# Kernel optimization log

Hardware: AMD Instinct MI355X
Metric: run time of the kernel (lower is better)

The kernel has to match this reference:

```python
import jax, jax.numpy as jnp
import numpy as np

N_NODES = 100_000
N_EDGES = 1_600_000
D_IN = 128
D_OUT = 128


def setup_inputs() -> dict:
    key = jax.random.key(0)
    k1, k2, k3, k4, k5 = jax.random.split(key, 5)
    feature = jax.random.normal(k1, (N_NODES, D_IN), dtype=jnp.float32)
    W = jax.random.normal(k2, (D_IN, D_OUT), dtype=jnp.float32) * 0.05
    b = jax.random.normal(k3, (D_OUT,), dtype=jnp.float32) * 0.05
    src = jax.random.randint(k4, (N_EDGES,), 0, N_NODES, dtype=jnp.int32)
    dst = jax.random.randint(k5, (N_EDGES,), 0, N_NODES, dtype=jnp.int32)
    return {"feature": feature, "W": W, "b": b, "src": src, "dst": dst}


def reference(feature, W, b, src, dst):
    N = feature.shape[0]
    # in-degrees (number of incoming edges per node)
    in_deg = jax.ops.segment_sum(
        jnp.ones(dst.shape[0], dtype=feature.dtype), dst, num_segments=N
    )  # [N]
    # degree-constraint scaling: h = x / sqrt(in_deg + 1)
    feat = feature * (1.0 / jnp.sqrt(in_deg + 1.0))[:, None]  # [N, D]
    # copy_u messages + mean reduce over incoming edges
    msg = feat[src]  # [E, D]
    summed = jax.ops.segment_sum(msg, dst, num_segments=N)  # [N, D]
    cnt = in_deg[:, None]
    h = jnp.where(cnt > 0, summed / jnp.maximum(cnt, 1.0), 0.0)  # DGL mean -> 0 for isolated nodes
    # apply_mod linear
    return h @ W + b
```

## Files before the change

kernel.cpp:

```cpp
#include <hip/hip_runtime.h>
#include <math.h>


#define D 128
#define MT 32
#define CPAD 16
#define INL 15
#define CAPT 48
#define SCAP 33

typedef short short8 __attribute__((ext_vector_type(8)));
typedef float f32x4 __attribute__((ext_vector_type(4)));

__device__ inline unsigned short f2b(float f) {
    unsigned u = __float_as_uint(f);
    return (unsigned short)((u + 0x7FFFu + ((u >> 16) & 1u)) >> 16);
}
#define B2F(u) __uint_as_float(((unsigned)(u)) << 16)

__global__ __launch_bounds__(256) void k_fill(const int* __restrict__ src,
                                              const int* __restrict__ dst,
                                              int* __restrict__ cl,
                                              int* __restrict__ spill,
                                              int ne, int nn) {
#define PUT(s_, d_) { int p = atomicAdd(&cl[(d_) * CPAD], 1);                  \
        if (p < INL) cl[(d_) * CPAD + 1 + p] = (s_);                           \
        else if (p < CAPT) spill[(size_t)(d_) * SCAP + (p - INL)] = (s_); }
    int i = blockIdx.x * 256 + threadIdx.x;
    int e0 = i * 4;
    if (e0 + 4 <= ne) {
        int4 sv = ((const int4*)src)[i];
        int4 dv = ((const int4*)dst)[i];
        PUT(sv.x, dv.x)
        PUT(sv.y, dv.y)
        PUT(sv.z, dv.z)
        PUT(sv.w, dv.w)
    } else {
        for (int e = e0; e < ne; ++e) PUT(src[e], dst[e])
    }
#undef PUT
}

__global__ __launch_bounds__(256) void k_mid(const int* __restrict__ cl,
                                             const float* __restrict__ W,
                                             float* __restrict__ scale,
                                             unsigned short* __restrict__ Wt,
                                             int nn, int sb) {
    int t = threadIdx.x;
    if (blockIdx.x < sb) {
        int n = blockIdx.x * 256 + t;
        if (n < nn) scale[n] = rsqrtf((float)cl[n * CPAD] + 1.0f);
        return;
    }
    int d = t & 127, k0 = (t >> 7) * 64;
    for (int k = 0; k < 64; ++k)
        Wt[d * D + k0 + k] = f2b(W[(size_t)(k0 + k) * D + d]);
}

__global__ __launch_bounds__(256) void k_gemm(const float* __restrict__ feature,
                                              const unsigned short* __restrict__ Wt,
                                              unsigned short* __restrict__ Yb,
                                              int nn) {
    int t = threadIdx.x;
    int w = t >> 6, l = t & 63;
    int rg = w & 1, ch = w >> 1;
    int base = blockIdx.x * MT;
    int r = base + rg * 16 + (l & 15);
    if (r >= nn) r = nn - 1;
    int kl = (l >> 4) * 8;

    short8 af[4];
    const float* fr = feature + (size_t)r * D;
#pragma unroll
    for (int kc = 0; kc < 4; ++kc) {
        float4 x = *(const float4*)(fr + kc * 32 + kl);
        float4 y = *(const float4*)(fr + kc * 32 + kl + 4);
        short8 a;
        a[0] = (short)f2b(x.x); a[1] = (short)f2b(x.y);
        a[2] = (short)f2b(x.z); a[3] = (short)f2b(x.w);
        a[4] = (short)f2b(y.x); a[5] = (short)f2b(y.y);
        a[6] = (short)f2b(y.z); a[7] = (short)f2b(y.w);
        af[kc] = a;
    }

    f32x4 acc[4];
#pragma unroll
    for (int ct = 0; ct < 4; ++ct) acc[ct] = (f32x4){0.f, 0.f, 0.f, 0.f};

#pragma unroll
    for (int ct = 0; ct < 4; ++ct) {
        int c = ch * 64 + ct * 16 + (l & 15);
        const unsigned short* wr = Wt + (size_t)c * D;
#pragma unroll
        for (int kc = 0; kc < 4; ++kc) {
            short8 b = *(const short8*)(wr + kc * 32 + kl);
            acc[ct] = __builtin_amdgcn_mfma_f32_16x16x32_bf16(af[kc], b, acc[ct], 0, 0, 0);
        }
    }

#pragma unroll
    for (int ct = 0; ct < 4; ++ct) {
        int c = ch * 64 + ct * 16 + (l & 15);
        int r0 = base + rg * 16 + (l >> 4) * 4;
#pragma unroll
        for (int j = 0; j < 4; ++j) {
            int row = r0 + j;
            if (row < nn) Yb[(size_t)row * D + c] = f2b(acc[ct][j]);
        }
    }
}

__global__ __launch_bounds__(256) void k_agg(const unsigned short* __restrict__ Yb,
                                             const float* __restrict__ bias,
                                             const int* __restrict__ cl,
                                             const int* __restrict__ spill,
                                             const float* __restrict__ scale,
                                             float* __restrict__ out,
                                             int n_nodes) {
    int t = threadIdx.x;
    int wave = t >> 6, lane = t & 63;
    int hw = lane >> 5, sl = lane & 31;
    int base = blockIdx.x * MT;

    const ushort4* y4 = (const ushort4*)Yb;
    float4 bv = ((const float4*)bias)[sl];

#pragma unroll
    for (int j = 0; j < 4; ++j) {
        int n = base + wave * 8 + j * 2 + hw;
        bool valid = (n < n_nodes);
        int nc = valid ? n : 0;
        int lv;
        if (sl < 16) lv = cl[nc * CPAD + sl];
        else         lv = spill[(size_t)nc * SCAP + (sl - 16)];
        int c = __shfl(lv, 0, 32);
        if (!valid) c = 0;
        if (c > CAPT) c = CAPT;
        float4 a0 = make_float4(0.f, 0.f, 0.f, 0.f), a1 = a0, a2 = a0, a3 = a0;
        if (c > 0) {
            int iv0 = ((unsigned)lv < (unsigned)n_nodes) ? lv : 0;
            float sv0 = scale[iv0];
            int nv = c < 31 ? c : 31;
            int e = 0;
            for (; e + 8 <= nv; e += 8) {
                int i0 = __shfl(iv0, e + 1, 32), i1 = __shfl(iv0, e + 2, 32);
                int i2 = __shfl(iv0, e + 3, 32), i3 = __shfl(iv0, e + 4, 32);
                int i4 = __shfl(iv0, e + 5, 32), i5 = __shfl(iv0, e + 6, 32);
                int i6 = __shfl(iv0, e + 7, 32), i7 = __shfl(iv0, e + 8, 32);
                float c0 = __shfl(sv0, e + 1, 32), c1 = __shfl(sv0, e + 2, 32);
                float c2 = __shfl(sv0, e + 3, 32), c3 = __shfl(sv0, e + 4, 32);
                float c4 = __shfl(sv0, e + 5, 32), c5 = __shfl(sv0, e + 6, 32);
                float c6 = __shfl(sv0, e + 7, 32), c7 = __shfl(sv0, e + 8, 32);
                ushort4 u0 = y4[(size_t)i0 * 32 + sl], u1 = y4[(size_t)i1 * 32 + sl];
                ushort4 u2 = y4[(size_t)i2 * 32 + sl], u3 = y4[(size_t)i3 * 32 + sl];
                ushort4 u4 = y4[(size_t)i4 * 32 + sl], u5 = y4[(size_t)i5 * 32 + sl];
                ushort4 u6 = y4[(size_t)i6 * 32 + sl], u7 = y4[(size_t)i7 * 32 + sl];
                a0.x = fmaf(B2F(u0.x), c0, a0.x); a0.y = fmaf(B2F(u0.y), c0, a0.y);
                a0.z = fmaf(B2F(u0.z), c0, a0.z); a0.w = fmaf(B2F(u0.w), c0, a0.w);
                a1.x = fmaf(B2F(u1.x), c1, a1.x); a1.y = fmaf(B2F(u1.y), c1, a1.y);
                a1.z = fmaf(B2F(u1.z), c1, a1.z); a1.w = fmaf(B2F(u1.w), c1, a1.w);
                a2.x = fmaf(B2F(u2.x), c2, a2.x); a2.y = fmaf(B2F(u2.y), c2, a2.y);
                a2.z = fmaf(B2F(u2.z), c2, a2.z); a2.w = fmaf(B2F(u2.w), c2, a2.w);
                a3.x = fmaf(B2F(u3.x), c3, a3.x); a3.y = fmaf(B2F(u3.y), c3, a3.y);
                a3.z = fmaf(B2F(u3.z), c3, a3.z); a3.w = fmaf(B2F(u3.w), c3, a3.w);
                a0.x = fmaf(B2F(u4.x), c4, a0.x); a0.y = fmaf(B2F(u4.y), c4, a0.y);
                a0.z = fmaf(B2F(u4.z), c4, a0.z); a0.w = fmaf(B2F(u4.w), c4, a0.w);
                a1.x = fmaf(B2F(u5.x), c5, a1.x); a1.y = fmaf(B2F(u5.y), c5, a1.y);
                a1.z = fmaf(B2F(u5.z), c5, a1.z); a1.w = fmaf(B2F(u5.w), c5, a1.w);
                a2.x = fmaf(B2F(u6.x), c6, a2.x); a2.y = fmaf(B2F(u6.y), c6, a2.y);
                a2.z = fmaf(B2F(u6.z), c6, a2.z); a2.w = fmaf(B2F(u6.w), c6, a2.w);
                a3.x = fmaf(B2F(u7.x), c7, a3.x); a3.y = fmaf(B2F(u7.y), c7, a3.y);
                a3.z = fmaf(B2F(u7.z), c7, a3.z); a3.w = fmaf(B2F(u7.w), c7, a3.w);
            }
            for (; e + 4 <= nv; e += 4) {
                int i0 = __shfl(iv0, e + 1, 32), i1 = __shfl(iv0, e + 2, 32);
                int i2 = __shfl(iv0, e + 3, 32), i3 = __shfl(iv0, e + 4, 32);
                float c0 = __shfl(sv0, e + 1, 32), c1 = __shfl(sv0, e + 2, 32);
                float c2 = __shfl(sv0, e + 3, 32), c3 = __shfl(sv0, e + 4, 32);
                ushort4 u0 = y4[(size_t)i0 * 32 + sl], u1 = y4[(size_t)i1 * 32 + sl];
                ushort4 u2 = y4[(size_t)i2 * 32 + sl], u3 = y4[(size_t)i3 * 32 + sl];
                a0.x = fmaf(B2F(u0.x), c0, a0.x); a0.y = fmaf(B2F(u0.y), c0, a0.y);
                a0.z = fmaf(B2F(u0.z), c0, a0.z); a0.w = fmaf(B2F(u0.w), c0, a0.w);
                a1.x = fmaf(B2F(u1.x), c1, a1.x); a1.y = fmaf(B2F(u1.y), c1, a1.y);
                a1.z = fmaf(B2F(u1.z), c1, a1.z); a1.w = fmaf(B2F(u1.w), c1, a1.w);
                a2.x = fmaf(B2F(u2.x), c2, a2.x); a2.y = fmaf(B2F(u2.y), c2, a2.y);
                a2.z = fmaf(B2F(u2.z), c2, a2.z); a2.w = fmaf(B2F(u2.w), c2, a2.w);
                a3.x = fmaf(B2F(u3.x), c3, a3.x); a3.y = fmaf(B2F(u3.y), c3, a3.y);
                a3.z = fmaf(B2F(u3.z), c3, a3.z); a3.w = fmaf(B2F(u3.w), c3, a3.w);
            }
            for (; e < nv; ++e) {
                int s = __shfl(iv0, e + 1, 32);
                float cc = __shfl(sv0, e + 1, 32);
                ushort4 u = y4[(size_t)s * 32 + sl];
                a0.x = fmaf(B2F(u.x), cc, a0.x); a0.y = fmaf(B2F(u.y), cc, a0.y);
                a0.z = fmaf(B2F(u.z), cc, a0.z); a0.w = fmaf(B2F(u.w), cc, a0.w);
            }
            for (int p = 31; p < c; ++p) {
                int s = spill[(size_t)nc * SCAP + (p - INL)];
                s = ((unsigned)s < (unsigned)n_nodes) ? s : 0;
                float cc = scale[s];
                ushort4 u = y4[(size_t)s * 32 + sl];
                a0.x = fmaf(B2F(u.x), cc, a0.x); a0.y = fmaf(B2F(u.y), cc, a0.y);
                a0.z = fmaf(B2F(u.z), cc, a0.z); a0.w = fmaf(B2F(u.w), cc, a0.w);
            }
        }
        if (valid) {
            float invn = (c > 0) ? (1.0f / (float)c) : 0.f;
            float4 r;
            r.x = (a0.x + a1.x + a2.x + a3.x) * invn + bv.x;
            r.y = (a0.y + a1.y + a2.y + a3.y) * invn + bv.y;
            r.z = (a0.z + a1.z + a2.z + a3.z) * invn + bv.z;
            r.w = (a0.w + a1.w + a2.w + a3.w) * invn + bv.w;
            ((float4*)out)[(size_t)n * 32 + sl] = r;
        }
    }
}

extern "C" void kernel_launch(void* const* d_in, const int* in_sizes, int n_in,
                              void* d_out, int out_size, void* d_ws, size_t ws_size,
                              hipStream_t stream) {
    const float* feature = (const float*)d_in[0];
    const float* W = (const float*)d_in[1];
    const float* bias = (const float*)d_in[2];
    const int* src = (const int*)d_in[3];
    const int* dst = (const int*)d_in[4];
    float* out = (float*)d_out;

    int n_nodes = in_sizes[0] / D;
    int n_edges = in_sizes[3];
    (void)n_in; (void)out_size; (void)ws_size;

    char* ws = (char*)d_ws;
    size_t o = 0;
    auto alloc = [&](size_t bytes) { void* p = ws + o; o += (bytes + 511) & ~(size_t)511; return p; };
    int* cl = (int*)alloc((size_t)n_nodes * CPAD * 4);
    int* spill = (int*)alloc((size_t)n_nodes * SCAP * 4);
    unsigned short* Yb = (unsigned short*)alloc((size_t)n_nodes * D * 2);
    float* scale = (float*)alloc((size_t)n_nodes * 4);
    unsigned short* Wt = (unsigned short*)alloc((size_t)D * D * 2);

    hipMemsetAsync(cl, 0, (size_t)n_nodes * CPAD * 4, stream);

    int fb = (n_edges + 1023) / 1024;
    int sb = (n_nodes + 255) / 256;
    int tiles = (n_nodes + MT - 1) / MT;

    k_fill<<<fb, 256, 0, stream>>>(src, dst, cl, spill, n_edges, n_nodes);
    k_mid<<<sb + 1, 256, 0, stream>>>(cl, W, scale, Wt, n_nodes, sb);
    k_gemm<<<tiles, 256, 0, stream>>>(feature, Wt, Yb, n_nodes);
    k_agg<<<tiles, 256, 0, stream>>>(Yb, bias, cl, spill, scale, out, n_nodes);
}
```

Before: 291.0 us.

## Fold source-degree scaling into GEMM epilogue and drop per-edge scale gathers

Moves the 1/sqrt(in_deg+1) source scaling out of the aggregation loop and applies it to each row of Y in the GEMM epilogue, using the linearity of the matmul. Aggregation then does plain bf16 adds with no per-edge scale gather or shuffle, the scale array and its kernel pass go away, and spill-list loads are skipped for low-degree nodes. In exchange the scale is applied before bf16 rounding of Y, which changes rounding slightly, and k_gemm now has to read the count array.

```diff
diff --git a/kernel.cpp b/kernel.cpp
--- a/kernel.cpp
+++ b/kernel.cpp
@@ -41,17 +41,9 @@
 #undef PUT
 }
 
-__global__ __launch_bounds__(256) void k_mid(const int* __restrict__ cl,
-                                             const float* __restrict__ W,
-                                             float* __restrict__ scale,
-                                             unsigned short* __restrict__ Wt,
-                                             int nn, int sb) {
+__global__ __launch_bounds__(256) void k_mid(const float* __restrict__ W,
+                                             unsigned short* __restrict__ Wt) {
     int t = threadIdx.x;
-    if (blockIdx.x < sb) {
-        int n = blockIdx.x * 256 + t;
-        if (n < nn) scale[n] = rsqrtf((float)cl[n * CPAD] + 1.0f);
-        return;
-    }
     int d = t & 127, k0 = (t >> 7) * 64;
     for (int k = 0; k < 64; ++k)
         Wt[d * D + k0 + k] = f2b(W[(size_t)(k0 + k) * D + d]);
@@ -59,6 +51,7 @@
 
 __global__ __launch_bounds__(256) void k_gemm(const float* __restrict__ feature,
                                               const unsigned short* __restrict__ Wt,
+                                              const int* __restrict__ cl,
                                               unsigned short* __restrict__ Yb,
                                               int nn) {
     int t = threadIdx.x;
@@ -98,14 +91,21 @@
         }
     }
 
+    int r0 = base + rg * 16 + (l >> 4) * 4;
+    float sc[4];
+#pragma unroll
+    for (int j = 0; j < 4; ++j) {
+        int row = (r0 + j < nn) ? (r0 + j) : (nn - 1);
+        sc[j] = rsqrtf((float)cl[row * CPAD] + 1.0f);
+    }
+
 #pragma unroll
     for (int ct = 0; ct < 4; ++ct) {
         int c = ch * 64 + ct * 16 + (l & 15);
-        int r0 = base + rg * 16 + (l >> 4) * 4;
 #pragma unroll
         for (int j = 0; j < 4; ++j) {
             int row = r0 + j;
-            if (row < nn) Yb[(size_t)row * D + c] = f2b(acc[ct][j]);
+            if (row < nn) Yb[(size_t)row * D + c] = f2b(acc[ct][j] * sc[j]);
         }
     }
 }
@@ -114,7 +114,6 @@
                                              const float* __restrict__ bias,
                                              const int* __restrict__ cl,
                                              const int* __restrict__ spill,
-                                             const float* __restrict__ scale,
                                              float* __restrict__ out,
                                              int n_nodes) {
     int t = threadIdx.x;
@@ -130,16 +129,15 @@
         int n = base + wave * 8 + j * 2 + hw;
         bool valid = (n < n_nodes);
         int nc = valid ? n : 0;
-        int lv;
-        if (sl < 16) lv = cl[nc * CPAD + sl];
-        else         lv = spill[(size_t)nc * SCAP + (sl - 16)];
+        int lv = cl[nc * CPAD + (sl & 15)];
         int c = __shfl(lv, 0, 32);
         if (!valid) c = 0;
         if (c > CAPT) c = CAPT;
+        if (c > INL && sl >= 16)
+            lv = spill[(size_t)nc * SCAP + (sl - 16)];
         float4 a0 = make_float4(0.f, 0.f, 0.f, 0.f), a1 = a0, a2 = a0, a3 = a0;
         if (c > 0) {
             int iv0 = ((unsigned)lv < (unsigned)n_nodes) ? lv : 0;
-            float sv0 = scale[iv0];
             int nv = c < 31 ? c : 31;
             int e = 0;
             for (; e + 8 <= nv; e += 8) {
@@ -147,61 +145,39 @@
                 int i2 = __shfl(iv0, e + 3, 32), i3 = __shfl(iv0, e + 4, 32);
                 int i4 = __shfl(iv0, e + 5, 32), i5 = __shfl(iv0, e + 6, 32);
                 int i6 = __shfl(iv0, e + 7, 32), i7 = __shfl(iv0, e + 8, 32);
-                float c0 = __shfl(sv0, e + 1, 32), c1 = __shfl(sv0, e + 2, 32);
-                float c2 = __shfl(sv0, e + 3, 32), c3 = __shfl(sv0, e + 4, 32);
-                float c4 = __shfl(sv0, e + 5, 32), c5 = __shfl(sv0, e + 6, 32);
-                float c6 = __shfl(sv0, e + 7, 32), c7 = __shfl(sv0, e + 8, 32);
                 ushort4 u0 = y4[(size_t)i0 * 32 + sl], u1 = y4[(size_t)i1 * 32 + sl];
                 ushort4 u2 = y4[(size_t)i2 * 32 + sl], u3 = y4[(size_t)i3 * 32 + sl];
                 ushort4 u4 = y4[(size_t)i4 * 32 + sl], u5 = y4[(size_t)i5 * 32 + sl];
                 ushort4 u6 = y4[(size_t)i6 * 32 + sl], u7 = y4[(size_t)i7 * 32 + sl];
-                a0.x = fmaf(B2F(u0.x), c0, a0.x); a0.y = fmaf(B2F(u0.y), c0, a0.y);
-                a0.z = fmaf(B2F(u0.z), c0, a0.z); a0.w = fmaf(B2F(u0.w), c0, a0.w);
-                a1.x = fmaf(B2F(u1.x), c1, a1.x); a1.y = fmaf(B2F(u1.y), c1, a1.y);
-                a1.z = fmaf(B2F(u1.z), c1, a1.z); a1.w = fmaf(B2F(u1.w), c1, a1.w);
-                a2.x = fmaf(B2F(u2.x), c2, a2.x); a2.y = fmaf(B2F(u2.y), c2, a2.y);
-                a2.z = fmaf(B2F(u2.z), c2, a2.z); a2.w = fmaf(B2F(u2.w), c2, a2.w);
-                a3.x = fmaf(B2F(u3.x), c3, a3.x); a3.y = fmaf(B2F(u3.y), c3, a3.y);
-                a3.z = fmaf(B2F(u3.z), c3, a3.z); a3.w = fmaf(B2F(u3.w), c3, a3.w);
-                a0.x = fmaf(B2F(u4.x), c4, a0.x); a0.y = fmaf(B2F(u4.y), c4, a0.y);
-                a0.z = fmaf(B2F(u4.z), c4, a0.z); a0.w = fmaf(B2F(u4.w), c4, a0.w);
-                a1.x = fmaf(B2F(u5.x), c5, a1.x); a1.y = fmaf(B2F(u5.y), c5, a1.y);
-                a1.z = fmaf(B2F(u5.z), c5, a1.z); a1.w = fmaf(B2F(u5.w), c5, a1.w);
-                a2.x = fmaf(B2F(u6.x), c6, a2.x); a2.y = fmaf(B2F(u6.y), c6, a2.y);
-                a2.z = fmaf(B2F(u6.z), c6, a2.z); a2.w = fmaf(B2F(u6.w), c6, a2.w);
-                a3.x = fmaf(B2F(u7.x), c7, a3.x); a3.y = fmaf(B2F(u7.y), c7, a3.y);
-                a3.z = fmaf(B2F(u7.z), c7, a3.z); a3.w = fmaf(B2F(u7.w), c7, a3.w);
+                a0.x += B2F(u0.x); a0.y += B2F(u0.y); a0.z += B2F(u0.z); a0.w += B2F(u0.w);
+                a1.x += B2F(u1.x); a1.y += B2F(u1.y); a1.z += B2F(u1.z); a1.w += B2F(u1.w);
+                a2.x += B2F(u2.x); a2.y += B2F(u2.y); a2.z += B2F(u2.z); a2.w += B2F(u2.w);
+                a3.x += B2F(u3.x); a3.y += B2F(u3.y); a3.z += B2F(u3.z); a3.w += B2F(u3.w);
+                a0.x += B2F(u4.x); a0.y += B2F(u4.y); a0.z += B2F(u4.z); a0.w += B2F(u4.w);
+                a1.x += B2F(u5.x); a1.y += B2F(u5.y); a1.z += B2F(u5.z); a1.w += B2F(u5.w);
+                a2.x += B2F(u6.x); a2.y += B2F(u6.y); a2.z += B2F(u6.z); a2.w += B2F(u6.w);
+                a3.x += B2F(u7.x); a3.y += B2F(u7.y); a3.z += B2F(u7.z); a3.w += B2F(u7.w);
             }
             for (; e + 4 <= nv; e += 4) {
                 int i0 = __shfl(iv0, e + 1, 32), i1 = __shfl(iv0, e + 2, 32);
                 int i2 = __shfl(iv0, e + 3, 32), i3 = __shfl(iv0, e + 4, 32);
-                float c0 = __shfl(sv0, e + 1, 32), c1 = __shfl(sv0, e + 2, 32);
-                float c2 = __shfl(sv0, e + 3, 32), c3 = __shfl(sv0, e + 4, 32);
                 ushort4 u0 = y4[(size_t)i0 * 32 + sl], u1 = y4[(size_t)i1 * 32 + sl];
                 ushort4 u2 = y4[(size_t)i2 * 32 + sl], u3 = y4[(size_t)i3 * 32 + sl];
-                a0.x = fmaf(B2F(u0.x), c0, a0.x); a0.y = fmaf(B2F(u0.y), c0, a0.y);
-                a0.z = fmaf(B2F(u0.z), c0, a0.z); a0.w = fmaf(B2F(u0.w), c0, a0.w);
-                a1.x = fmaf(B2F(u1.x), c1, a1.x); a1.y = fmaf(B2F(u1.y), c1, a1.y);
-                a1.z = fmaf(B2F(u1.z), c1, a1.z); a1.w = fmaf(B2F(u1.w), c1, a1.w);
-                a2.x = fmaf(B2F(u2.x), c2, a2.x); a2.y = fmaf(B2F(u2.y), c2, a2.y);
-                a2.z = fmaf(B2F(u2.z), c2, a2.z); a2.w = fmaf(B2F(u2.w), c2, a2.w);
-                a3.x = fmaf(B2F(u3.x), c3, a3.x); a3.y = fmaf(B2F(u3.y), c3, a3.y);
-                a3.z = fmaf(B2F(u3.z), c3, a3.z); a3.w = fmaf(B2F(u3.w), c3, a3.w);
+                a0.x += B2F(u0.x); a0.y += B2F(u0.y); a0.z += B2F(u0.z); a0.w += B2F(u0.w);
+                a1.x += B2F(u1.x); a1.y += B2F(u1.y); a1.z += B2F(u1.z); a1.w += B2F(u1.w);
+                a2.x += B2F(u2.x); a2.y += B2F(u2.y); a2.z += B2F(u2.z); a2.w += B2F(u2.w);
+                a3.x += B2F(u3.x); a3.y += B2F(u3.y); a3.z += B2F(u3.z); a3.w += B2F(u3.w);
             }
             for (; e < nv; ++e) {
                 int s = __shfl(iv0, e + 1, 32);
-                float cc = __shfl(sv0, e + 1, 32);
                 ushort4 u = y4[(size_t)s * 32 + sl];
-                a0.x = fmaf(B2F(u.x), cc, a0.x); a0.y = fmaf(B2F(u.y), cc, a0.y);
-                a0.z = fmaf(B2F(u.z), cc, a0.z); a0.w = fmaf(B2F(u.w), cc, a0.w);
+                a0.x += B2F(u.x); a0.y += B2F(u.y); a0.z += B2F(u.z); a0.w += B2F(u.w);
             }
             for (int p = 31; p < c; ++p) {
                 int s = spill[(size_t)nc * SCAP + (p - INL)];
                 s = ((unsigned)s < (unsigned)n_nodes) ? s : 0;
-                float cc = scale[s];
                 ushort4 u = y4[(size_t)s * 32 + sl];
-                a0.x = fmaf(B2F(u.x), cc, a0.x); a0.y = fmaf(B2F(u.y), cc, a0.y);
-                a0.z = fmaf(B2F(u.z), cc, a0.z); a0.w = fmaf(B2F(u.w), cc, a0.w);
+                a0.x += B2F(u.x); a0.y += B2F(u.y); a0.z += B2F(u.z); a0.w += B2F(u.w);
             }
         }
         if (valid) {
@@ -236,17 +212,15 @@
     int* cl = (int*)alloc((size_t)n_nodes * CPAD * 4);
     int* spill = (int*)alloc((size_t)n_nodes * SCAP * 4);
     unsigned short* Yb = (unsigned short*)alloc((size_t)n_nodes * D * 2);
-    float* scale = (float*)alloc((size_t)n_nodes * 4);
     unsigned short* Wt = (unsigned short*)alloc((size_t)D * D * 2);
 
     hipMemsetAsync(cl, 0, (size_t)n_nodes * CPAD * 4, stream);
 
     int fb = (n_edges + 1023) / 1024;
-    int sb = (n_nodes + 255) / 256;
     int tiles = (n_nodes + MT - 1) / MT;
 
     k_fill<<<fb, 256, 0, stream>>>(src, dst, cl, spill, n_edges, n_nodes);
-    k_mid<<<sb + 1, 256, 0, stream>>>(cl, W, scale, Wt, n_nodes, sb);
-    k_gemm<<<tiles, 256, 0, stream>>>(feature, Wt, Yb, n_nodes);
-    k_agg<<<tiles, 256, 0, stream>>>(Yb, bias, cl, spill, scale, out, n_nodes);
-}
+    k_mid<<<1, 256, 0, stream>>>(W, Wt);
+    k_gemm<<<tiles, 256, 0, stream>>>(feature, Wt, cl, Yb, n_nodes);
+    k_agg<<<tiles, 256, 0, stream>>>(Yb, bias, cl, spill, out, n_nodes);
+}
```

After: 288.9 us. About the same (-0.7%).

## Fuse edge bucketing with GEMM in one launch and fold memset into prep kernel

Applied to the files above, without the earlier changes.

The hipMemset is replaced by a prep kernel that zeroes the per-node bucket array and also transposes W to bf16. Edge bucketing and the feature GEMM now run as separate block ranges of a single launch, so the atomic-heavy fill can overlap with the MFMA work. Scale computation moves to its own small kernel. The aggregation kernel reads the spill list only for nodes whose in-degree exceeds the inline capacity, which avoids most spill-row loads. The trade-off is one extra small launch and contention between the two workloads sharing the GPU.

```diff
diff --git a/kernel.cpp b/kernel.cpp
--- a/kernel.cpp
+++ b/kernel.cpp
@@ -18,53 +18,53 @@
 }
 #define B2F(u) __uint_as_float(((unsigned)(u)) << 16)
 
-__global__ __launch_bounds__(256) void k_fill(const int* __restrict__ src,
-                                              const int* __restrict__ dst,
-                                              int* __restrict__ cl,
-                                              int* __restrict__ spill,
-                                              int ne, int nn) {
+__global__ __launch_bounds__(256) void k_prep(const float* __restrict__ W,
+                                              unsigned short* __restrict__ Wt,
+                                              int4* __restrict__ cl4,
+                                              int nz4) {
+    int t = threadIdx.x;
+    if (blockIdx.x == 0) {
+        int d = t & 127, k0 = (t >> 7) * 64;
+        for (int k = 0; k < 64; ++k)
+            Wt[d * D + k0 + k] = f2b(W[(size_t)(k0 + k) * D + d]);
+        return;
+    }
+    int i = (blockIdx.x - 1) * 256 + t;
+    if (i < nz4) cl4[i] = make_int4(0, 0, 0, 0);
+}
+
+__global__ __launch_bounds__(256) void k_fg(const int* __restrict__ src,
+                                            const int* __restrict__ dst,
+                                            const float* __restrict__ feature,
+                                            const unsigned short* __restrict__ Wt,
+                                            int* __restrict__ cl,
+                                            int* __restrict__ spill,
+                                            unsigned short* __restrict__ Yb,
+                                            int ne, int nn, int fb) {
+    int t = threadIdx.x;
+    if (blockIdx.x < fb) {
 #define PUT(s_, d_) { int p = atomicAdd(&cl[(d_) * CPAD], 1);                  \
         if (p < INL) cl[(d_) * CPAD + 1 + p] = (s_);                           \
         else if (p < CAPT) spill[(size_t)(d_) * SCAP + (p - INL)] = (s_); }
-    int i = blockIdx.x * 256 + threadIdx.x;
-    int e0 = i * 4;
-    if (e0 + 4 <= ne) {
-        int4 sv = ((const int4*)src)[i];
-        int4 dv = ((const int4*)dst)[i];
-        PUT(sv.x, dv.x)
-        PUT(sv.y, dv.y)
-        PUT(sv.z, dv.z)
-        PUT(sv.w, dv.w)
-    } else {
-        for (int e = e0; e < ne; ++e) PUT(src[e], dst[e])
-    }
+        int i = blockIdx.x * 256 + t;
+        int e0 = i * 4;
+        if (e0 + 4 <= ne) {
+            int4 sv = ((const int4*)src)[i];
+            int4 dv = ((const int4*)dst)[i];
+            PUT(sv.x, dv.x)
+            PUT(sv.y, dv.y)
+            PUT(sv.z, dv.z)
+            PUT(sv.w, dv.w)
+        } else {
+            for (int e = e0; e < ne; ++e) PUT(src[e], dst[e])
+        }
 #undef PUT
-}
-
-__global__ __launch_bounds__(256) void k_mid(const int* __restrict__ cl,
-                                             const float* __restrict__ W,
-                                             float* __restrict__ scale,
-                                             unsigned short* __restrict__ Wt,
-                                             int nn, int sb) {
-    int t = threadIdx.x;
-    if (blockIdx.x < sb) {
-        int n = blockIdx.x * 256 + t;
-        if (n < nn) scale[n] = rsqrtf((float)cl[n * CPAD] + 1.0f);
         return;
     }
-    int d = t & 127, k0 = (t >> 7) * 64;
-    for (int k = 0; k < 64; ++k)
-        Wt[d * D + k0 + k] = f2b(W[(size_t)(k0 + k) * D + d]);
-}
-
-__global__ __launch_bounds__(256) void k_gemm(const float* __restrict__ feature,
-                                              const unsigned short* __restrict__ Wt,
-                                              unsigned short* __restrict__ Yb,
-                                              int nn) {
-    int t = threadIdx.x;
+
     int w = t >> 6, l = t & 63;
     int rg = w & 1, ch = w >> 1;
-    int base = blockIdx.x * MT;
+    int base = (blockIdx.x - fb) * MT;
     int r = base + rg * 16 + (l & 15);
     if (r >= nn) r = nn - 1;
     int kl = (l >> 4) * 8;
@@ -108,6 +108,13 @@
             if (row < nn) Yb[(size_t)row * D + c] = f2b(acc[ct][j]);
         }
     }
+}
+
+__global__ __launch_bounds__(256) void k_scale(const int* __restrict__ cl,
+                                               float* __restrict__ scale,
+                                               int nn) {
+    int n = blockIdx.x * 256 + threadIdx.x;
+    if (n < nn) scale[n] = rsqrtf((float)cl[n * CPAD] + 1.0f);
 }
 
 __global__ __launch_bounds__(256) void k_agg(const unsigned short* __restrict__ Yb,
@@ -130,12 +137,12 @@
         int n = base + wave * 8 + j * 2 + hw;
         bool valid = (n < n_nodes);
         int nc = valid ? n : 0;
-        int lv;
-        if (sl < 16) lv = cl[nc * CPAD + sl];
-        else         lv = spill[(size_t)nc * SCAP + (sl - 16)];
+        int lv = cl[nc * CPAD + (sl & 15)];
         int c = __shfl(lv, 0, 32);
         if (!valid) c = 0;
         if (c > CAPT) c = CAPT;
+        if (c > INL && sl >= 16)
+            lv = spill[(size_t)nc * SCAP + (sl - 16)];
         float4 a0 = make_float4(0.f, 0.f, 0.f, 0.f), a1 = a0, a2 = a0, a3 = a0;
         if (c > 0) {
             int iv0 = ((unsigned)lv < (unsigned)n_nodes) ? lv : 0;
@@ -239,14 +246,15 @@
     float* scale = (float*)alloc((size_t)n_nodes * 4);
     unsigned short* Wt = (unsigned short*)alloc((size_t)D * D * 2);
 
-    hipMemsetAsync(cl, 0, (size_t)n_nodes * CPAD * 4, stream);
-
+    int nz4 = n_nodes * CPAD / 4;
+    int zb = (nz4 + 255) / 256;
     int fb = (n_edges + 1023) / 1024;
     int sb = (n_nodes + 255) / 256;
     int tiles = (n_nodes + MT - 1) / MT;
 
-    k_fill<<<fb, 256, 0, stream>>>(src, dst, cl, spill, n_edges, n_nodes);
-    k_mid<<<sb + 1, 256, 0, stream>>>(cl, W, scale, Wt, n_nodes, sb);
-    k_gemm<<<tiles, 256, 0, stream>>>(feature, Wt, Yb, n_nodes);
+    k_prep<<<zb + 1, 256, 0, stream>>>(W, Wt, (int4*)cl, nz4);
+    k_fg<<<fb + tiles, 256, 0, stream>>>(src, dst, feature, Wt, cl, spill, Yb,
+                                         n_edges, n_nodes, fb);
+    k_scale<<<sb, 256, 0, stream>>>(cl, scale, n_nodes);
     k_agg<<<tiles, 256, 0, stream>>>(Yb, bias, cl, spill, scale, out, n_nodes);
 }
```

Measured after the change: 292.1 us. No clear change (+0.4%).
